# Kernel tuning notes

Measured on AMD Instinct MI355X. Metric: run time of the kernel, lower is better.

## Reference

```python
import jax, jax.numpy as jnp
import numpy as np

D_MODEL = 1024
NUM_HEADS = 16
D_K = D_MODEL // NUM_HEADS


def setup_inputs() -> dict:
    key = jax.random.key(0)
    ks = jax.random.split(key, 5)
    x = jax.random.normal(ks[0], (8, 1024, D_MODEL), dtype=jnp.float32)
    s_in = 1.0 / np.sqrt(D_MODEL)
    W_qkv = jax.random.normal(ks[1], (D_MODEL, 3 * D_MODEL), dtype=jnp.float32) * s_in
    b_qkv = jax.random.normal(ks[2], (3 * D_MODEL,), dtype=jnp.float32) * 0.01
    W_o = jax.random.normal(ks[3], (D_MODEL, D_MODEL), dtype=jnp.float32) * s_in
    b_o = jax.random.normal(ks[4], (D_MODEL,), dtype=jnp.float32) * 0.01
    return {"x": x, "W_qkv": W_qkv, "b_qkv": b_qkv, "W_o": W_o, "b_o": b_o}


def reference(x, W_qkv, b_qkv, W_o, b_o):
    B, N, D = x.shape
    qkv = x @ W_qkv + b_qkv                      # [B, N, 3D]
    qkv = qkv.reshape(B, N, 3, NUM_HEADS, D_K)
    qkv = jnp.transpose(qkv, (2, 0, 3, 1, 4))    # [3, B, H, N, d_k]
    q, k, v = qkv[0], qkv[1], qkv[2]
    scale = 1.0 / np.sqrt(D_K).astype(np.float32)
    attn = jnp.einsum('bhqd,bhkd->bhqk', q, k) * scale
    attn = jax.nn.softmax(attn, axis=-1)
    out = jnp.einsum('bhqk,bhkd->bhqd', attn, v)  # [B, H, N, d_k]
    out = jnp.transpose(out, (0, 2, 1, 3)).reshape(B, N, D)
    return out @ W_o + b_o
```

## Files before the change

### kernel.cpp

```cpp
#include <hip/hip_runtime.h>


typedef __attribute__((ext_vector_type(8))) short bf16x8;
typedef __attribute__((ext_vector_type(4))) float f32x4;

#define GLOAD_LDS16(gp, lp)                                                              \
  __builtin_amdgcn_global_load_lds((const __attribute__((address_space(1))) void*)(gp),  \
                                   (__attribute__((address_space(3))) void*)(lp), 16, 0, 0)

__device__ __forceinline__ unsigned short f2bf(float f) {
  unsigned int u = __float_as_uint(f);
  u += 0x7fffu + ((u >> 16) & 1u);
  return (unsigned short)(u >> 16);
}

__global__ __launch_bounds__(256) void prep_fused(
    const float* __restrict__ x, unsigned short* __restrict__ x_bf,
    const float* __restrict__ W_qkv, unsigned short* __restrict__ wqkv_t,
    const float* __restrict__ W_o, unsigned short* __restrict__ wo_t) {
  const int b = blockIdx.x;
  if (b < 2048) {
    const int n4 = 8388608 / 4;
    for (int i = b * 256 + threadIdx.x; i < n4; i += 2048 * 256) {
      float4 v = reinterpret_cast<const float4*>(x)[i];
      ushort4 o;
      o.x = f2bf(v.x); o.y = f2bf(v.y); o.z = f2bf(v.z); o.w = f2bf(v.w);
      reinterpret_cast<ushort4*>(x_bf)[i] = o;
    }
  } else {
    __shared__ float tile[32][33];
    const float* W;
    unsigned short* Wt;
    int R = 1024, C, bx, by;
    if (b < 5120) {
      W = W_qkv; Wt = wqkv_t; C = 3072;
      int bb = b - 2048; bx = bb % 96; by = bb / 96;
    } else {
      W = W_o; Wt = wo_t; C = 1024;
      int bb = b - 5120; bx = bb & 31; by = bb >> 5;
    }
    const int tx = threadIdx.x & 31, ty = threadIdx.x >> 5;
    const int c0 = bx * 32, r0 = by * 32;
    #pragma unroll
    for (int i = 0; i < 4; i++) {
      int r = r0 + ty + i * 8;
      tile[ty + i * 8][tx] = W[(size_t)r * C + c0 + tx];
    }
    __syncthreads();
    #pragma unroll
    for (int i = 0; i < 4; i++) {
      int c = c0 + ty + i * 8;
      Wt[(size_t)c * R + r0 + tx] = f2bf(tile[tx][ty + i * 8]);
    }
  }
}

template <int MODE>
__global__ __launch_bounds__(512) void gemm256(
    const unsigned short* __restrict__ A, const unsigned short* __restrict__ Bt,
    const float* __restrict__ bias, unsigned short* __restrict__ qkv_out,
    float* __restrict__ Cout) {
  __shared__ __align__(16) unsigned short As[3][128 * 64];
  __shared__ __align__(16) unsigned short Bs[3][256 * 64];
  const int t = threadIdx.x;
  const int lane = t & 63, wid = t >> 6;
  const int lr = lane & 15, g = lane >> 4;
  const int wm = wid >> 2, wn = wid & 3;

  const int nwg = gridDim.x * gridDim.y;
  const int id = blockIdx.x + gridDim.x * blockIdx.y;
  const int sw = (id & 7) * (nwg >> 3) + (id >> 3);
  const int bx = sw % gridDim.x, by = sw / gridDim.x;
  const int row0 = by * 128, col0 = bx * 256;

  const int srow = t >> 3, sch = t & 7;

  auto stA = [&](int buf, int kt, int j) {
    int row = j * 64 + srow;
    int ch = sch ^ (row & 7);
    GLOAD_LDS16(A + (size_t)(row0 + row) * 1024 + kt * 64 + ch * 8,
                (char*)&As[buf][0] + j * 8192 + t * 16);
  };
  auto stB = [&](int buf, int kt, int j) {
    int row = j * 64 + srow;
    int ch = sch ^ (row & 7);
    GLOAD_LDS16(Bt + (size_t)(col0 + row) * 1024 + kt * 64 + ch * 8,
                (char*)&Bs[buf][0] + j * 8192 + t * 16);
  };
  auto rdA = [&](int buf, int c, int m) -> bf16x8 {
    int r = wm * 64 + m * 16 + lr;
    return *(const bf16x8*)((const char*)&As[buf][0] + r * 128 +
                            ((c * 64 + g * 16) ^ ((r & 7) << 4)));
  };
  auto rdB = [&](int buf, int c, int n) -> bf16x8 {
    int r = wn * 64 + n * 16 + lr;
    return *(const bf16x8*)((const char*)&Bs[buf][0] + r * 128 +
                            ((c * 64 + g * 16) ^ ((r & 7) << 4)));
  };

  f32x4 acc[4][4] = {};

  stA(0, 0, 0); stA(0, 0, 1);
  stB(0, 0, 0); stB(0, 0, 1); stB(0, 0, 2); stB(0, 0, 3);
  stA(1, 1, 0); stA(1, 1, 1);
  stB(1, 1, 0); stB(1, 1, 1); stB(1, 1, 2); stB(1, 1, 3);

  for (int kt = 0; kt < 16; kt++) {
    const int buf = kt % 3;
    const int bufn = (kt + 2) % 3;
    const bool pf = (kt <= 13);

    if (kt == 15) asm volatile("s_waitcnt vmcnt(0)" ::: "memory");
    else          asm volatile("s_waitcnt vmcnt(6)" ::: "memory");
    __builtin_amdgcn_s_barrier();
    __builtin_amdgcn_sched_barrier(0);

    bf16x8 a0[4], b0[4];
    #pragma unroll
    for (int m = 0; m < 4; m++) a0[m] = rdA(buf, 0, m);
    #pragma unroll
    for (int n = 0; n < 4; n++) b0[n] = rdB(buf, 0, n);
    if (pf) { stA(bufn, kt + 2, 0); stA(bufn, kt + 2, 1); stB(bufn, kt + 2, 0); }
    #pragma unroll
    for (int m = 0; m < 4; m++)
      #pragma unroll
      for (int n = 0; n < 4; n++)
        acc[m][n] = __builtin_amdgcn_mfma_f32_16x16x32_bf16(a0[m], b0[n], acc[m][n], 0, 0, 0);

    bf16x8 a1[4], b1[4];
    #pragma unroll
    for (int m = 0; m < 4; m++) a1[m] = rdA(buf, 1, m);
    #pragma unroll
    for (int n = 0; n < 4; n++) b1[n] = rdB(buf, 1, n);
    if (pf) { stB(bufn, kt + 2, 1); stB(bufn, kt + 2, 2); stB(bufn, kt + 2, 3); }
    #pragma unroll
    for (int m = 0; m < 4; m++)
      #pragma unroll
      for (int n = 0; n < 4; n++)
        acc[m][n] = __builtin_amdgcn_mfma_f32_16x16x32_bf16(a1[m], b1[n], acc[m][n], 0, 0, 0);
  }

  if (MODE == 0) {
    const int which = col0 >> 10;
    if (which == 2) {
      #pragma unroll
      for (int m = 0; m < 4; m++) {
        int row = row0 + wm * 64 + m * 16 + g * 4;
        int bb = row >> 10, nn = row & 1023;
        #pragma unroll
        for (int n = 0; n < 4; n++) {
          int col = col0 + wn * 64 + n * 16 + lr;
          int cc = col & 1023;
          int h = cc >> 6, dk = cc & 63;
          float bv = bias[col];
          ushort4 w;
          w.x = f2bf(acc[m][n][0] + bv);
          w.y = f2bf(acc[m][n][1] + bv);
          w.z = f2bf(acc[m][n][2] + bv);
          w.w = f2bf(acc[m][n][3] + bv);
          size_t idx = ((size_t)2 << 23) + (((size_t)(bb * 16 + h)) << 16) +
                       (size_t)dk * 1024 + nn;
          *(ushort4*)(qkv_out + idx) = w;
        }
      }
    } else {
      #pragma unroll
      for (int m = 0; m < 4; m++) {
        #pragma unroll
        for (int n = 0; n < 4; n++) {
          int col = col0 + wn * 64 + n * 16 + lr;
          int cc = col & 1023;
          int h = cc >> 6, dk = cc & 63;
          #pragma unroll
          for (int r = 0; r < 4; r++) {
            int row = row0 + wm * 64 + m * 16 + g * 4 + r;
            int bb = row >> 10, nn = row & 1023;
            float v = acc[m][n][r] + bias[col];
            if (which == 0) v *= 0.125f;
            size_t idx = ((size_t)which << 23) +
                         (((size_t)((bb * 16 + h) * 1024 + nn)) << 6) + dk;
            qkv_out[idx] = f2bf(v);
          }
        }
      }
    }
  } else {
    #pragma unroll
    for (int m = 0; m < 4; m++) {
      #pragma unroll
      for (int n = 0; n < 4; n++) {
        int col = col0 + wn * 64 + n * 16 + lr;
        #pragma unroll
        for (int r = 0; r < 4; r++) {
          int row = row0 + wm * 64 + m * 16 + g * 4 + r;
          Cout[(size_t)row * 1024 + col] = acc[m][n][r] + bias[col];
        }
      }
    }
  }
}

__global__ __launch_bounds__(512) void attn_mfma(
    const unsigned short* __restrict__ qkv, unsigned short* __restrict__ attn_out) {
  __shared__ __align__(16) unsigned short K_lds[2][64 * 64];
  __shared__ __align__(16) unsigned short V_lds[2][64 * 64];
  __shared__ __align__(16) unsigned short P_lds[128 * 64];

  const int bid = ((blockIdx.x & 7) << 7) + (blockIdx.x >> 3);
  const int bh = bid >> 3, qt = bid & 7;
  const unsigned short* Qp = qkv + ((size_t)bh << 16);
  const unsigned short* Kp = qkv + (1u << 23) + ((size_t)bh << 16);
  const unsigned short* Vt = qkv + (2u << 23) + ((size_t)bh << 16);

  const int t = threadIdx.x;
  const int lane = t & 63, wid = t >> 6;
  const int lr = lane & 15, g = lane >> 4;

  bf16x8 qf[2];
  {
    int qrow = qt * 128 + wid * 16 + lr;
    qf[0] = *(const bf16x8*)(Qp + (size_t)qrow * 64 + g * 8);
    qf[1] = *(const bf16x8*)(Qp + (size_t)qrow * 64 + 32 + g * 8);
  }

  const int srow = t >> 3;
  const int sch  = (t & 7) ^ (srow & 7);
  const int so   = t * 16;

  auto stage = [&](int buf, int kt) {
    GLOAD_LDS16(Kp + (size_t)(kt * 64 + srow) * 64 + sch * 8, (char*)&K_lds[buf][0] + so);
    GLOAD_LDS16(Vt + (size_t)srow * 1024 + kt * 64 + sch * 8, (char*)&V_lds[buf][0] + so);
  };

  f32x4 o_acc[4] = {};
  float den_l = 0.f;
  const int qrow_w = wid * 16 + lr;

  stage(0, 0);
  __syncthreads();
  int buf = 0;
  for (int kt = 0; kt < 16; kt++) {
    if (kt + 1 < 16) stage(buf ^ 1, kt + 1);

    f32x4 s4[4] = {};
    __builtin_amdgcn_s_setprio(1);
    #pragma unroll
    for (int ks = 0; ks < 4; ks++) {
      int krow = ks * 16 + lr;
      #pragma unroll
      for (int c = 0; c < 2; c++) {
        bf16x8 kf = *(const bf16x8*)((char*)&K_lds[buf][0] + krow * 128 +
                                     ((c * 64 + g * 16) ^ ((krow & 7) << 4)));
        s4[ks] = __builtin_amdgcn_mfma_f32_16x16x32_bf16(kf, qf[c], s4[ks], 0, 0, 0);
      }
    }
    __builtin_amdgcn_s_setprio(0);

    #pragma unroll
    for (int ks = 0; ks < 4; ks++) {
      float e0 = __expf(s4[ks][0]);
      float e1 = __expf(s4[ks][1]);
      float e2 = __expf(s4[ks][2]);
      float e3 = __expf(s4[ks][3]);
      den_l += (e0 + e1) + (e2 + e3);
      unsigned int lo = (unsigned int)f2bf(e0) | ((unsigned int)f2bf(e1) << 16);
      unsigned int hi = (unsigned int)f2bf(e2) | ((unsigned int)f2bf(e3) << 16);
      int k0 = ks * 16 + g * 4;
      *(uint2*)((char*)P_lds + qrow_w * 128 +
                ((k0 * 2) ^ ((qrow_w & 7) << 4))) = make_uint2(lo, hi);
    }

    bf16x8 pa[2];
    {
      int q = wid * 16 + lr;
      #pragma unroll
      for (int c = 0; c < 2; c++)
        pa[c] = *(const bf16x8*)((char*)P_lds + q * 128 +
                                 ((c * 64 + g * 16) ^ ((q & 7) << 4)));
    }
    __builtin_amdgcn_s_setprio(1);
    #pragma unroll
    for (int ds_ = 0; ds_ < 4; ds_++) {
      int drow = ds_ * 16 + lr;
      #pragma unroll
      for (int c = 0; c < 2; c++) {
        bf16x8 vf = *(const bf16x8*)((char*)&V_lds[buf][0] + drow * 128 +
                                     ((c * 64 + g * 16) ^ ((drow & 7) << 4)));
        o_acc[ds_] = __builtin_amdgcn_mfma_f32_16x16x32_bf16(pa[c], vf, o_acc[ds_], 0, 0, 0);
      }
    }
    __builtin_amdgcn_s_setprio(0);
    __syncthreads();
    buf ^= 1;
  }

  den_l += __shfl_xor(den_l, 16, 64);
  den_l += __shfl_xor(den_l, 32, 64);
  float den_r[4];
  #pragma unroll
  for (int r = 0; r < 4; r++) den_r[r] = __shfl(den_l, g * 4 + r, 64);

  const int bb = bh >> 4, h = bh & 15;
  #pragma unroll
  for (int ds_ = 0; ds_ < 4; ds_++) {
    #pragma unroll
    for (int r = 0; r < 4; r++) {
      int q = qt * 128 + wid * 16 + g * 4 + r;
      int d = h * 64 + ds_ * 16 + lr;
      attn_out[((size_t)(bb * 1024 + q)) * 1024 + d] = f2bf(o_acc[ds_][r] / den_r[r]);
    }
  }
}

extern "C" void kernel_launch(void* const* d_in, const int* in_sizes, int n_in,
                              void* d_out, int out_size, void* d_ws, size_t ws_size,
                              hipStream_t stream) {
  const float* x     = (const float*)d_in[0];
  const float* W_qkv = (const float*)d_in[1];
  const float* b_qkv = (const float*)d_in[2];
  const float* W_o   = (const float*)d_in[3];
  const float* b_o   = (const float*)d_in[4];
  float* out = (float*)d_out;

  unsigned short* ws      = (unsigned short*)d_ws;
  unsigned short* x_bf    = ws;
  unsigned short* wqkv_t  = x_bf + 8388608;
  unsigned short* wo_t    = wqkv_t + 3145728;
  unsigned short* qkv     = wo_t + 1048576;
  unsigned short* attn_o  = qkv + 25165824;

  prep_fused<<<6144, 256, 0, stream>>>(x, x_bf, W_qkv, wqkv_t, W_o, wo_t);
  gemm256<0><<<dim3(12, 64), 512, 0, stream>>>(x_bf, wqkv_t, b_qkv, qkv, nullptr);
  attn_mfma<<<1024, 512, 0, stream>>>(qkv, attn_o);
  gemm256<1><<<dim3(4, 64), 512, 0, stream>>>(attn_o, wo_t, b_o, nullptr, out);
}
```

Before: 154.1 us.

## Replace 128x256 triple-buffered GEMM with 128x128 double-buffered K=32 tiles

Rewrites the projection GEMM to use 128x128 output tiles with 256 threads, K-step 32, and double buffering with a simple syncthreads-based pipeline, in place of 128x256 tiles, 512 threads, K-step 64 and three-stage buffering. The smaller shared-memory footprint and grid (twice as many blocks) aim to raise occupancy and cut tail imbalance. The cost is less data reuse per tile, twice as many barriers per K, and the loss of the fine-grained vmcnt-controlled prefetch overlap.

```diff
diff --git a/kernel.cpp b/kernel.cpp
--- a/kernel.cpp
+++ b/kernel.cpp
@@ -56,88 +56,66 @@
 }
 
 template <int MODE>
-__global__ __launch_bounds__(512) void gemm256(
+__global__ __launch_bounds__(256) void gemm97(
     const unsigned short* __restrict__ A, const unsigned short* __restrict__ Bt,
     const float* __restrict__ bias, unsigned short* __restrict__ qkv_out,
     float* __restrict__ Cout) {
-  __shared__ __align__(16) unsigned short As[3][128 * 64];
-  __shared__ __align__(16) unsigned short Bs[3][256 * 64];
+  __shared__ __align__(16) unsigned short As[2][128 * 32];
+  __shared__ __align__(16) unsigned short Bs[2][128 * 32];
   const int t = threadIdx.x;
   const int lane = t & 63, wid = t >> 6;
   const int lr = lane & 15, g = lane >> 4;
-  const int wm = wid >> 2, wn = wid & 3;
+  const int wm = wid >> 1, wn = wid & 1;
 
   const int nwg = gridDim.x * gridDim.y;
   const int id = blockIdx.x + gridDim.x * blockIdx.y;
   const int sw = (id & 7) * (nwg >> 3) + (id >> 3);
   const int bx = sw % gridDim.x, by = sw / gridDim.x;
-  const int row0 = by * 128, col0 = bx * 256;
-
-  const int srow = t >> 3, sch = t & 7;
+  const int row0 = by * 128, col0 = bx * 128;
+
+  const int srow = t >> 2;
+  const int sch  = (t & 3) ^ ((srow >> 1) & 3);
 
   auto stA = [&](int buf, int kt, int j) {
-    int row = j * 64 + srow;
-    int ch = sch ^ (row & 7);
-    GLOAD_LDS16(A + (size_t)(row0 + row) * 1024 + kt * 64 + ch * 8,
-                (char*)&As[buf][0] + j * 8192 + t * 16);
+    GLOAD_LDS16(A + (size_t)(row0 + j * 64 + srow) * 1024 + kt * 32 + sch * 8,
+                (char*)&As[buf][0] + j * 4096 + t * 16);
   };
   auto stB = [&](int buf, int kt, int j) {
-    int row = j * 64 + srow;
-    int ch = sch ^ (row & 7);
-    GLOAD_LDS16(Bt + (size_t)(col0 + row) * 1024 + kt * 64 + ch * 8,
-                (char*)&Bs[buf][0] + j * 8192 + t * 16);
-  };
-  auto rdA = [&](int buf, int c, int m) -> bf16x8 {
+    GLOAD_LDS16(Bt + (size_t)(col0 + j * 64 + srow) * 1024 + kt * 32 + sch * 8,
+                (char*)&Bs[buf][0] + j * 4096 + t * 16);
+  };
+  auto rdA = [&](int buf, int m) -> bf16x8 {
     int r = wm * 64 + m * 16 + lr;
-    return *(const bf16x8*)((const char*)&As[buf][0] + r * 128 +
-                            ((c * 64 + g * 16) ^ ((r & 7) << 4)));
-  };
-  auto rdB = [&](int buf, int c, int n) -> bf16x8 {
+    return *(const bf16x8*)((const char*)&As[buf][0] + r * 64 +
+                            ((g ^ ((r >> 1) & 3)) * 16));
+  };
+  auto rdB = [&](int buf, int n) -> bf16x8 {
     int r = wn * 64 + n * 16 + lr;
-    return *(const bf16x8*)((const char*)&Bs[buf][0] + r * 128 +
-                            ((c * 64 + g * 16) ^ ((r & 7) << 4)));
+    return *(const bf16x8*)((const char*)&Bs[buf][0] + r * 64 +
+                            ((g ^ ((r >> 1) & 3)) * 16));
   };
 
   f32x4 acc[4][4] = {};
 
-  stA(0, 0, 0); stA(0, 0, 1);
-  stB(0, 0, 0); stB(0, 0, 1); stB(0, 0, 2); stB(0, 0, 3);
-  stA(1, 1, 0); stA(1, 1, 1);
-  stB(1, 1, 0); stB(1, 1, 1); stB(1, 1, 2); stB(1, 1, 3);
-
-  for (int kt = 0; kt < 16; kt++) {
-    const int buf = kt % 3;
-    const int bufn = (kt + 2) % 3;
-    const bool pf = (kt <= 13);
-
-    if (kt == 15) asm volatile("s_waitcnt vmcnt(0)" ::: "memory");
-    else          asm volatile("s_waitcnt vmcnt(6)" ::: "memory");
-    __builtin_amdgcn_s_barrier();
-    __builtin_amdgcn_sched_barrier(0);
-
-    bf16x8 a0[4], b0[4];
-    #pragma unroll
-    for (int m = 0; m < 4; m++) a0[m] = rdA(buf, 0, m);
-    #pragma unroll
-    for (int n = 0; n < 4; n++) b0[n] = rdB(buf, 0, n);
-    if (pf) { stA(bufn, kt + 2, 0); stA(bufn, kt + 2, 1); stB(bufn, kt + 2, 0); }
+  stA(0, 0, 0); stA(0, 0, 1); stB(0, 0, 0); stB(0, 0, 1);
+
+  for (int kt = 0; kt < 32; kt++) {
+    const int buf = kt & 1;
+    __syncthreads();
+    if (kt + 1 < 32) {
+      stA(buf ^ 1, kt + 1, 0); stA(buf ^ 1, kt + 1, 1);
+      stB(buf ^ 1, kt + 1, 0); stB(buf ^ 1, kt + 1, 1);
+    }
+    bf16x8 a[4], b[4];
+    #pragma unroll
+    for (int m = 0; m < 4; m++) a[m] = rdA(buf, m);
+    #pragma unroll
+    for (int n = 0; n < 4; n++) b[n] = rdB(buf, n);
     #pragma unroll
     for (int m = 0; m < 4; m++)
       #pragma unroll
       for (int n = 0; n < 4; n++)
-        acc[m][n] = __builtin_amdgcn_mfma_f32_16x16x32_bf16(a0[m], b0[n], acc[m][n], 0, 0, 0);
-
-    bf16x8 a1[4], b1[4];
-    #pragma unroll
-    for (int m = 0; m < 4; m++) a1[m] = rdA(buf, 1, m);
-    #pragma unroll
-    for (int n = 0; n < 4; n++) b1[n] = rdB(buf, 1, n);
-    if (pf) { stB(bufn, kt + 2, 1); stB(bufn, kt + 2, 2); stB(bufn, kt + 2, 3); }
-    #pragma unroll
-    for (int m = 0; m < 4; m++)
-      #pragma unroll
-      for (int n = 0; n < 4; n++)
-        acc[m][n] = __builtin_amdgcn_mfma_f32_16x16x32_bf16(a1[m], b1[n], acc[m][n], 0, 0, 0);
+        acc[m][n] = __builtin_amdgcn_mfma_f32_16x16x32_bf16(a[m], b[n], acc[m][n], 0, 0, 0);
   }
 
   if (MODE == 0) {
@@ -330,7 +308,7 @@
   unsigned short* attn_o  = qkv + 25165824;
 
   prep_fused<<<6144, 256, 0, stream>>>(x, x_bf, W_qkv, wqkv_t, W_o, wo_t);
-  gemm256<0><<<dim3(12, 64), 512, 0, stream>>>(x_bf, wqkv_t, b_qkv, qkv, nullptr);
+  gemm97<0><<<dim3(24, 64), 256, 0, stream>>>(x_bf, wqkv_t, b_qkv, qkv, nullptr);
   attn_mfma<<<1024, 512, 0, stream>>>(qkv, attn_o);
-  gemm256<1><<<dim3(4, 64), 512, 0, stream>>>(attn_o, wo_t, b_o, nullptr, out);
-}
+  gemm97<1><<<dim3(8, 64), 256, 0, stream>>>(attn_o, wo_t, b_o, nullptr, out);
+}
```

New measurement: 182.2 us. 18.2% more time.

## Use 128x384 tiles with K=32 steps for the QKV projection GEMM

Applied to the files above, without the earlier changes.

Replaces the templated QKV GEMM with a dedicated kernel that computes 128x384 output tiles, launched as 512 workgroups instead of 768, using 32-wide K steps in a triple-buffered LDS pipeline with a new XOR swizzle. Each wave now holds a 4x6 grid of MFMA accumulators. The aim is more reuse of each A tile per load and a grid that fits the CU count in fewer waves. Since a tile can now span the Q/K/V boundary, the epilogue picks the Q/K/V layout per column. The trade-offs are more accumulator registers, one barrier per 32-wide K step instead of per 64, and shallower prefetch per step.

```diff
diff --git a/kernel.cpp b/kernel.cpp
--- a/kernel.cpp
+++ b/kernel.cpp
@@ -55,11 +55,108 @@
   }
 }
 
-template <int MODE>
-__global__ __launch_bounds__(512) void gemm256(
+__global__ __launch_bounds__(512) void gemm1_384(
     const unsigned short* __restrict__ A, const unsigned short* __restrict__ Bt,
-    const float* __restrict__ bias, unsigned short* __restrict__ qkv_out,
-    float* __restrict__ Cout) {
+    const float* __restrict__ bias, unsigned short* __restrict__ qkv_out) {
+  __shared__ __align__(16) unsigned short As[3][128 * 32];
+  __shared__ __align__(16) unsigned short Bs[3][384 * 32];
+  const int t = threadIdx.x;
+  const int lane = t & 63, wid = t >> 6;
+  const int lr = lane & 15, g = lane >> 4;
+  const int wm = wid >> 2, wn = wid & 3;
+
+  const int nwg = gridDim.x * gridDim.y;
+  const int id = blockIdx.x + gridDim.x * blockIdx.y;
+  const int sw = (id & 7) * (nwg >> 3) + (id >> 3);
+  const int bx = sw % gridDim.x, by = sw / gridDim.x;
+  const int row0 = by * 128, col0 = bx * 384;
+
+  const int srow = t >> 2;
+  const int sch  = (t & 3) ^ ((srow >> 1) & 3);
+
+  auto stA = [&](int buf, int kt) {
+    GLOAD_LDS16(A + (size_t)(row0 + srow) * 1024 + kt * 32 + sch * 8,
+                (char*)&As[buf][0] + t * 16);
+  };
+  auto stB = [&](int buf, int kt, int j) {
+    GLOAD_LDS16(Bt + (size_t)(col0 + j * 128 + srow) * 1024 + kt * 32 + sch * 8,
+                (char*)&Bs[buf][0] + j * 8192 + t * 16);
+  };
+  auto rdA = [&](int buf, int m) -> bf16x8 {
+    int r = wm * 64 + m * 16 + lr;
+    return *(const bf16x8*)((const char*)&As[buf][0] + r * 64 +
+                            ((g ^ ((r >> 1) & 3)) * 16));
+  };
+  auto rdB = [&](int buf, int n) -> bf16x8 {
+    int r = wn * 96 + n * 16 + lr;
+    return *(const bf16x8*)((const char*)&Bs[buf][0] + r * 64 +
+                            ((g ^ ((r >> 1) & 3)) * 16));
+  };
+
+  f32x4 acc[4][6] = {};
+
+  stA(0, 0); stB(0, 0, 0); stB(0, 0, 1); stB(0, 0, 2);
+  stA(1, 1); stB(1, 1, 0); stB(1, 1, 1); stB(1, 1, 2);
+
+  for (int kt = 0; kt < 32; kt++) {
+    const int buf = kt % 3;
+    const int bufn = (kt + 2) % 3;
+    const bool pf = (kt <= 29);
+
+    if (kt == 31) asm volatile("s_waitcnt vmcnt(0)" ::: "memory");
+    else          asm volatile("s_waitcnt vmcnt(4)" ::: "memory");
+    __builtin_amdgcn_s_barrier();
+    __builtin_amdgcn_sched_barrier(0);
+
+    bf16x8 a[4], b[6];
+    #pragma unroll
+    for (int m = 0; m < 4; m++) a[m] = rdA(buf, m);
+    #pragma unroll
+    for (int n = 0; n < 6; n++) b[n] = rdB(buf, n);
+    if (pf) { stA(bufn, kt + 2); stB(bufn, kt + 2, 0); stB(bufn, kt + 2, 1); stB(bufn, kt + 2, 2); }
+    #pragma unroll
+    for (int m = 0; m < 4; m++)
+      #pragma unroll
+      for (int n = 0; n < 6; n++)
+        acc[m][n] = __builtin_amdgcn_mfma_f32_16x16x32_bf16(a[m], b[n], acc[m][n], 0, 0, 0);
+  }
+
+  #pragma unroll
+  for (int m = 0; m < 4; m++) {
+    const int row = row0 + wm * 64 + m * 16 + g * 4;
+    const int bb = row >> 10, nn = row & 1023;
+    #pragma unroll
+    for (int n = 0; n < 6; n++) {
+      const int col = col0 + wn * 96 + n * 16 + lr;
+      const int which = col >> 10;
+      const int cc = col & 1023;
+      const int h = cc >> 6, dk = cc & 63;
+      const float bv = bias[col];
+      if (which == 2) {
+        ushort4 w;
+        w.x = f2bf(acc[m][n][0] + bv);
+        w.y = f2bf(acc[m][n][1] + bv);
+        w.z = f2bf(acc[m][n][2] + bv);
+        w.w = f2bf(acc[m][n][3] + bv);
+        size_t idx = ((size_t)2 << 23) + (((size_t)(bb * 16 + h)) << 16) +
+                     (size_t)dk * 1024 + nn;
+        *(ushort4*)(qkv_out + idx) = w;
+      } else {
+        const float sc = (which == 0) ? 0.125f : 1.0f;
+        #pragma unroll
+        for (int r = 0; r < 4; r++) {
+          size_t idx = ((size_t)which << 23) +
+                       (((size_t)((bb * 16 + h) * 1024 + nn + r)) << 6) + dk;
+          qkv_out[idx] = f2bf((acc[m][n][r] + bv) * sc);
+        }
+      }
+    }
+  }
+}
+
+__global__ __launch_bounds__(512) void gemm2_k(
+    const unsigned short* __restrict__ A, const unsigned short* __restrict__ Bt,
+    const float* __restrict__ bias, float* __restrict__ Cout) {
   __shared__ __align__(16) unsigned short As[3][128 * 64];
   __shared__ __align__(16) unsigned short Bs[3][256 * 64];
   const int t = threadIdx.x;
@@ -140,61 +237,15 @@
         acc[m][n] = __builtin_amdgcn_mfma_f32_16x16x32_bf16(a1[m], b1[n], acc[m][n], 0, 0, 0);
   }
 
-  if (MODE == 0) {
-    const int which = col0 >> 10;
-    if (which == 2) {
-      #pragma unroll
-      for (int m = 0; m < 4; m++) {
-        int row = row0 + wm * 64 + m * 16 + g * 4;
-        int bb = row >> 10, nn = row & 1023;
-        #pragma unroll
-        for (int n = 0; n < 4; n++) {
-          int col = col0 + wn * 64 + n * 16 + lr;
-          int cc = col & 1023;
-          int h = cc >> 6, dk = cc & 63;
-          float bv = bias[col];
-          ushort4 w;
-          w.x = f2bf(acc[m][n][0] + bv);
-          w.y = f2bf(acc[m][n][1] + bv);
-          w.z = f2bf(acc[m][n][2] + bv);
-          w.w = f2bf(acc[m][n][3] + bv);
-          size_t idx = ((size_t)2 << 23) + (((size_t)(bb * 16 + h)) << 16) +
-                       (size_t)dk * 1024 + nn;
-          *(ushort4*)(qkv_out + idx) = w;
-        }
-      }
-    } else {
-      #pragma unroll
-      for (int m = 0; m < 4; m++) {
-        #pragma unroll
-        for (int n = 0; n < 4; n++) {
-          int col = col0 + wn * 64 + n * 16 + lr;
-          int cc = col & 1023;
-          int h = cc >> 6, dk = cc & 63;
-          #pragma unroll
-          for (int r = 0; r < 4; r++) {
-            int row = row0 + wm * 64 + m * 16 + g * 4 + r;
-            int bb = row >> 10, nn = row & 1023;
-            float v = acc[m][n][r] + bias[col];
-            if (which == 0) v *= 0.125f;
-            size_t idx = ((size_t)which << 23) +
-                         (((size_t)((bb * 16 + h) * 1024 + nn)) << 6) + dk;
-            qkv_out[idx] = f2bf(v);
-          }
-        }
-      }
-    }
-  } else {
-    #pragma unroll
-    for (int m = 0; m < 4; m++) {
-      #pragma unroll
-      for (int n = 0; n < 4; n++) {
-        int col = col0 + wn * 64 + n * 16 + lr;
-        #pragma unroll
-        for (int r = 0; r < 4; r++) {
-          int row = row0 + wm * 64 + m * 16 + g * 4 + r;
-          Cout[(size_t)row * 1024 + col] = acc[m][n][r] + bias[col];
-        }
+  #pragma unroll
+  for (int m = 0; m < 4; m++) {
+    #pragma unroll
+    for (int n = 0; n < 4; n++) {
+      int col = col0 + wn * 64 + n * 16 + lr;
+      #pragma unroll
+      for (int r = 0; r < 4; r++) {
+        int row = row0 + wm * 64 + m * 16 + g * 4 + r;
+        Cout[(size_t)row * 1024 + col] = acc[m][n][r] + bias[col];
       }
     }
   }
@@ -330,7 +381,7 @@
   unsigned short* attn_o  = qkv + 25165824;
 
   prep_fused<<<6144, 256, 0, stream>>>(x, x_bf, W_qkv, wqkv_t, W_o, wo_t);
-  gemm256<0><<<dim3(12, 64), 512, 0, stream>>>(x_bf, wqkv_t, b_qkv, qkv, nullptr);
+  gemm1_384<<<dim3(8, 64), 512, 0, stream>>>(x_bf, wqkv_t, b_qkv, qkv);
   attn_mfma<<<1024, 512, 0, stream>>>(qkv, attn_o);
-  gemm256<1><<<dim3(4, 64), 512, 0, stream>>>(attn_o, wo_t, b_o, nullptr, out);
-}
+  gemm2_k<<<dim3(4, 64), 512, 0, stream>>>(attn_o, wo_t, b_o, out);
+}
```

New measurement: 153.4 us, median of 3. Within noise of the previous version (-0.4%).
